# Performance work log

Hardware: AMD Instinct MI355X
Metric: run time of the kernel (lower is better)

## Reference

```python
import jax, jax.numpy as jnp
import numpy as np

N, H, DK, DV, DFF, D = 2, 8, 32, 32, 512, 256
B, S = 2, 2048
MASK_VALUE = -1e-30
EPS = 1e-14  # K.epsilon()**2 with default epsilon 1e-7


def glorot(key, shape):
    fan_in, fan_out = shape[-2], shape[-1]
    limit = np.sqrt(6.0 / (fan_in + fan_out))
    return jax.random.uniform(key, shape, jnp.float32, -limit, limit)


def setup_inputs() -> dict:
    key = jax.random.key(0)
    ks = jax.random.split(key, 8)
    return {
        "x": jax.random.normal(ks[0], (B, S, D), jnp.float32),
        "mask": jnp.ones((B, S), jnp.float32),
        "Wq": glorot(ks[1], (N, H, D, DK)),
        "Wk": glorot(ks[2], (N, H, D, DK)),
        "Wv": glorot(ks[3], (N, H, D, DV)),
        "Wo": glorot(ks[4], (N, H * DV, D)),
        "W1": glorot(ks[5], (N, D, DFF)),
        "b1": jnp.zeros((N, DFF), jnp.float32),
        "W2": glorot(ks[6], (N, DFF, D)),
        "b2": jnp.zeros((N, D), jnp.float32),
        "gamma": jnp.ones((2 * N,), jnp.float32),
        "beta": jnp.zeros((2 * N,), jnp.float32),
    }


def _layernorm(x, g, b):
    mean = jnp.mean(x, axis=-1, keepdims=True)
    var = jnp.mean(jnp.square(x - mean), axis=-1, keepdims=True)
    return (x - mean) / jnp.sqrt(var + EPS) * g + b


def reference(x, mask, Wq, Wk, Wv, Wo, W1, b1, W2, b2, gamma, beta):
    m = mask[:, None, None, :]  # [B,1,1,S], multiplies score rows' key axis
    for i in range(N):
        # batched multi-head attention (no 1/sqrt(dk) scaling, faithful to source)
        q = jnp.einsum("bsd,hdk->bhsk", x, Wq[i])
        k = jnp.einsum("bsd,hdk->bhsk", x, Wk[i])
        v = jnp.einsum("bsd,hdv->bhsv", x, Wv[i])
        A = jnp.einsum("bhsk,bhtk->bhst", q, k)  # [B,H,S,S]
        A = m * A + (1.0 - m) * MASK_VALUE
        A = jax.nn.softmax(A, axis=-1)
        o = jnp.einsum("bhst,bhtv->bhsv", A, v)
        conc = o.transpose(0, 2, 1, 3).reshape(x.shape[0], x.shape[1], H * DV)
        x = x + conc @ Wo[i]
        x = _layernorm(x, gamma[2 * i], beta[2 * i])
        ffn = jax.nn.relu(x @ W1[i] + b1[i]) @ W2[i] + b2[i]
        x = x + ffn
        x = _layernorm(x, gamma[2 * i + 1], beta[2 * i + 1])
    return x
```

## Files before the change

kernel.cpp:

```cpp
#include <hip/hip_runtime.h>
#include <hip/hip_bf16.h>

#define NL 2
#define NH 8
#define DKk 32
#define DVv 32
#define DFF 512
#define DD 256
#define BB 2
#define SS 2048
#define MROWS (BB*SS)
#define LN_EPS 1e-14f
#define L2E 1.4426950408889634f
#define SOFT_SHIFT_L2E (50.0f*L2E)

typedef __hip_bfloat16 bf16;
typedef unsigned short us;
typedef short bf16x8 __attribute__((ext_vector_type(8)));
typedef float f32x4  __attribute__((ext_vector_type(4)));
typedef unsigned short us4 __attribute__((ext_vector_type(4)));

#define O_XF   256
#define O_QB   (O_XF+1048576)
#define O_KH   (O_QB+1048576)
#define O_KL   (O_KH+524288)
#define O_VT   (O_KL+524288)
#define O_XH   (O_VT+524288)
#define O_XL   (O_XH+524288)
#define O_OP   (O_XL+524288)
#define O_ML   (O_OP+2097152)
#define O_MASK (O_ML+65536)
#define O_B1   (O_MASK+4096)
#define O_B2   (O_B1+1024)
#define O_GM   (O_B2+512)
#define O_BT   (O_GM+4)
#define O_PREP (O_BT+4)
#define TAIL_TOTAL (4096+1024+512+4+4)
#define CONV_BLOCKS (512 + (TAIL_TOTAL+255)/256)
#define PREP_BLOCKS 512
#define PQH 0u
#define PQL 393216u
#define POH 786432u
#define POL 917504u
#define P1H 1048576u
#define P1L 1310720u
#define P2H 1572864u
#define P2L 1835008u

__device__ __forceinline__ float us2f(us u){
  unsigned int v = ((unsigned int)u) << 16; float f;
  __builtin_memcpy(&f, &v, 4); return f;
}
__device__ __forceinline__ us f2bf_rne(float f){
  unsigned int b = __float_as_uint(f);
  b += 0x7FFFu + ((b>>16)&1u);
  return (us)(b>>16);
}

#if __has_builtin(__builtin_amdgcn_exp2f)
#define EXP2F(x) __builtin_amdgcn_exp2f(x)
#else
#define EXP2F(x) exp2f(x)
#endif

#if __has_builtin(__builtin_amdgcn_cvt_pk_bf16_f32)
typedef __bf16 bf16x2_t __attribute__((ext_vector_type(2)));
__device__ __forceinline__ int pack_bf16(float a, float b){
  bf16x2_t r = __builtin_amdgcn_cvt_pk_bf16_f32(a, b);
  int i; __builtin_memcpy(&i, &r, 4); return i;
}
#else
__device__ __forceinline__ int pack_bf16(float a, float b){
  int b0 = __float_as_int(a) + 0x8000;
  int b1 = __float_as_int(b) + 0x8000;
  return (b1 & 0xFFFF0000) | ((int)((unsigned)b0 >> 16));
}
#endif

__device__ __forceinline__ void gl_lds16(const us* g, us* l){
  __builtin_amdgcn_global_load_lds(
    (const __attribute__((address_space(1))) unsigned int*)g,
    (__attribute__((address_space(3))) unsigned int*)l, 16, 0, 0);
}

__device__ __forceinline__ size_t xhl_idx(int row, int col){
  int rt = row>>6, rg = (row>>4)&3, L15 = row&15;
  int kc = col>>5, Q = (col>>3)&3, j = col&7;
  return ((size_t)(rt*8+kc))*2048 + rg*512 + Q*128 + L15*8 + j;
}

__device__ __forceinline__ float conv1(const void* src, size_t i, int flag){
  if(flag) return ((const float*)src)[i];
  return us2f(((const us*)src)[i]);
}

__device__ __forceinline__ void prep_b_raw(const void* W0, const void* W1v, const void* W2v,
                                           int baseoff, us* __restrict__ Bh, us* __restrict__ Bl,
                                           int Kd, int Nd, int qkv, int g, int flag)
{
  int total = (Kd/32)*(Nd/16)*64;
  if(g >= total) return;
  int lane = g & 63, fi = g >> 6;
  int ncN = Nd/16;
  int nc = fi % ncN, kc = fi / ncN;
  int Q = lane>>4, L15 = lane&15;
  int n = nc*16 + L15;
  const void* src;
  int off0, stride;
  if(qkv){
    int sec = n>>8, h = (n>>5)&7, kq = n&31;
    src = (sec==0)?W0:((sec==1)?W1v:W2v);
    off0 = baseoff + h*8192 + kq;
    stride = 32;
  } else {
    src = W0;
    off0 = baseoff + n;
    stride = Nd;
  }
  #pragma unroll
  for(int j=0;j<8;j++){
    int k = kc*32 + Q*8 + j;
    float v = conv1(src, (size_t)off0 + (size_t)k*stride, flag);
    us hb = f2bf_rne(v);
    Bh[(size_t)g*8 + j] = hb;
    Bl[(size_t)g*8 + j] = f2bf_rne(v - us2f(hb));
  }
}

__global__ void conv_prep(const void* s0, const void* s1, const void* sWq, const void* sWk,
                          const void* sWv, const void* sWo, const void* sW1, const void* sb1,
                          const void* sW2, const void* sb2, const void* sgm, const void* sbt,
                          float* __restrict__ ws, int* __restrict__ flagp)
{
  __shared__ int fsh[4];
  int bad = 0;
  const us* xr = (const us*)s0;
  for(int i=threadIdx.x; i<4096; i+=256){
    float f = us2f(xr[i]);
    if(!(fabsf(f) < 1e3f)) bad = 1;
  }
  unsigned long long m = __ballot(bad);
  if((threadIdx.x&63)==0) fsh[threadIdx.x>>6] = (m!=0ull);
  __syncthreads();
  int flag = (fsh[0]|fsh[1]|fsh[2]|fsh[3]);
  if(blockIdx.x==0 && threadIdx.x==0) *flagp = flag;

  int b = blockIdx.x;
  if(b < PREP_BLOCKS){
    int layer = b >> 8, lb = b & 255;
    us* prep = (us*)(ws + O_PREP);
    if(lb < 96){
      int g = lb*256 + threadIdx.x;
      prep_b_raw(sWq, sWk, sWv, layer*65536, prep+PQH+(size_t)layer*196608,
                 prep+PQL+(size_t)layer*196608, 256, 768, 1, g, flag);
    } else if(lb < 128){
      int g = (lb-96)*256 + threadIdx.x;
      prep_b_raw(sWo, nullptr, nullptr, layer*65536, prep+POH+(size_t)layer*65536,
                 prep+POL+(size_t)layer*65536, 256, 256, 0, g, flag);
    } else if(lb < 192){
      int g = (lb-128)*256 + threadIdx.x;
      prep_b_raw(sW1, nullptr, nullptr, layer*131072, prep+P1H+(size_t)layer*131072,
                 prep+P1L+(size_t)layer*131072, 256, 512, 0, g, flag);
    } else {
      int g = (lb-192)*256 + threadIdx.x;
      prep_b_raw(sW2, nullptr, nullptr, layer*131072, prep+P2H+(size_t)layer*131072,
                 prep+P2L+(size_t)layer*131072, 512, 256, 0, g, flag);
    }
    return;
  }
  int b2 = b - PREP_BLOCKS;
  if(b2 < 512){
    int g8 = b2*256 + threadIdx.x;
    int e0 = g8*8;
    float v[8];
    if(flag){
      float4 a0 = *((const float4*)s0 + (e0>>2));
      float4 a1 = *((const float4*)s0 + (e0>>2) + 1);
      v[0]=a0.x; v[1]=a0.y; v[2]=a0.z; v[3]=a0.w;
      v[4]=a1.x; v[5]=a1.y; v[6]=a1.z; v[7]=a1.w;
    } else {
      bf16x8 u = *((const bf16x8*)s0 + g8);
      #pragma unroll
      for(int j=0;j<8;j++) v[j] = us2f((us)u[j]);
    }
    *(float4*)&ws[O_XF+e0]   = (float4){v[0],v[1],v[2],v[3]};
    *(float4*)&ws[O_XF+e0+4] = (float4){v[4],v[5],v[6],v[7]};
    union{ us a[8]; uint4 q; } hh, ll;
    #pragma unroll
    for(int j=0;j<8;j++){
      us hb = f2bf_rne(v[j]);
      hh.a[j] = hb;
      ll.a[j] = f2bf_rne(v[j] - us2f(hb));
    }
    size_t xi = xhl_idx(e0>>8, e0&255);
    *(uint4*)&((us*)(ws+O_XH))[xi] = hh.q;
    *(uint4*)&((us*)(ws+O_XL))[xi] = ll.q;
    return;
  }
  int g = (b2-512)*256 + threadIdx.x;
  if(g < 4096){ ws[O_MASK+g] = conv1(s1, g, flag)*L2E; return; }
  g -= 4096;
  if(g < 1024){ ws[O_B1+g] = conv1(sb1, g, flag); return; }
  g -= 1024;
  if(g < 512){ ws[O_B2+g] = conv1(sb2, g, flag); return; }
  g -= 512;
  if(g < 4){ ws[O_GM+g] = conv1(sgm, g, flag); return; }
  g -= 4;
  if(g < 4){ ws[O_BT+g] = conv1(sbt, g, flag); return; }
}

template<int MODE>
__launch_bounds__(256)
__global__ void gemm_mfma(const us* __restrict__ Axh, const us* __restrict__ Axl,
                          const us* __restrict__ Bh, const us* __restrict__ Bl,
                          const float* __restrict__ bias,
                          float* __restrict__ O,
                          us* __restrict__ QH, us* __restrict__ QL,
                          us* __restrict__ KH, us* __restrict__ KL, us* __restrict__ VT,
                          int Ncols, int Kdim)
{
  __shared__ __align__(16) us SH[16384];
  const int t = threadIdx.x;
  const int w = t>>6, lane = t&63;
  const int Q = lane>>4, L15 = lane&15;
  const int bx = blockIdx.x, by = blockIdx.y;
  const int row0 = bx*64;
  const int nc0 = by*4;
  const int col0 = by*64;
  const int nKc = Kdim>>5;
  const int ncW = Ncols>>4;

  f32x4 acc[2][2];
  #pragma unroll
  for(int i=0;i<2;i++)
    #pragma unroll
    for(int j=0;j<2;j++) acc[i][j] = (f32x4){0.f,0.f,0.f,0.f};

  auto stage = [&](int kc){
    const int bo = (kc&1)*8192;
    size_t abase = ((size_t)(bx*nKc + kc))*2048;
    gl_lds16(&Axh[abase + (size_t)t*8], &SH[bo + t*8]);
    gl_lds16(&Axl[abase + (size_t)t*8], &SH[bo + 2048 + t*8]);
    size_t gidx = ((size_t)(kc*ncW + nc0 + w)*64 + lane)*8;
    gl_lds16(&Bh[gidx], &SH[bo + 4096 + t*8]);
    gl_lds16(&Bl[gidx], &SH[bo + 6144 + t*8]);
  };

  stage(0);

  for(int kc=0; kc<nKc; kc++){
    __syncthreads();
    if(kc+1 < nKc) stage(kc+1);
    const int bo = (kc&1)*8192;
    const us* Ah  = SH + bo;
    const us* Al  = SH + bo + 2048;
    const us* Bhs = SH + bo + 4096;
    const us* Bls = SH + bo + 6144;

    bf16x8 aAh[2], aAl[2], bBh[2], bBl[2];
    #pragma unroll
    for(int rg2=0;rg2<2;rg2++){
      int rg = (w&1)*2 + rg2;
      aAh[rg2] = *(const bf16x8*)&Ah[rg*512 + lane*8];
      aAl[rg2] = *(const bf16x8*)&Al[rg*512 + lane*8];
    }
    #pragma unroll
    for(int cg2=0;cg2<2;cg2++){
      int nc = (w>>1)*2 + cg2;
      bBh[cg2] = *(const bf16x8*)&Bhs[nc*512 + lane*8];
      bBl[cg2] = *(const bf16x8*)&Bls[nc*512 + lane*8];
    }
    #pragma unroll
    for(int rg2=0;rg2<2;rg2++)
      #pragma unroll
      for(int cg2=0;cg2<2;cg2++){
        acc[rg2][cg2] = __builtin_amdgcn_mfma_f32_16x16x32_bf16(aAl[rg2], bBh[cg2], acc[rg2][cg2], 0,0,0);
        acc[rg2][cg2] = __builtin_amdgcn_mfma_f32_16x16x32_bf16(aAh[rg2], bBl[cg2], acc[rg2][cg2], 0,0,0);
        acc[rg2][cg2] = __builtin_amdgcn_mfma_f32_16x16x32_bf16(aAh[rg2], bBh[cg2], acc[rg2][cg2], 0,0,0);
      }
  }

  if(MODE==0){
    __syncthreads();
    us* TH = SH;
    us* TL = SH + 4608;
    #pragma unroll
    for(int rg2=0;rg2<2;rg2++)
      #pragma unroll
      for(int cg2=0;cg2<2;cg2++)
        #pragma unroll
        for(int r=0;r<4;r++){
          int rl = (w&1)*32 + rg2*16 + Q*4 + r;
          int cl = (w>>1)*32 + cg2*16 + L15;
          float va = acc[rg2][cg2][r];
          us hb = f2bf_rne(va);
          TH[rl*72+cl] = hb;
          TL[rl*72+cl] = f2bf_rne(va - us2f(hb));
        }
    __syncthreads();
    const int sec = col0>>8;
    const int h0  = (col0&255)>>5;
    const int b_  = row0>>11;
    const int srow0 = row0 & 2047;
    if(sec < 2){
      us* DH = (sec==0) ? QH : KH;
      us* DL = (sec==0) ? QL : KL;
      #pragma unroll
      for(int u2=0; u2<2; u2++){
        int u = w + u2*4;
        int rg = u&3, half = u>>2;
        int lbase = (rg*16 + L15)*72 + half*32 + Q*8;
        bf16x8 hv = *(const bf16x8*)&TH[lbase];
        bf16x8 lv = *(const bf16x8*)&TL[lbase];
        int bh = b_*NH + h0 + half;
        size_t dbase = ((size_t)(bh*128 + (srow0>>4) + rg)*64 + lane)*8;
        *(bf16x8*)&DH[dbase] = hv;
        *(bf16x8*)&DL[dbase] = lv;
      }
    } else {
      #pragma unroll
      for(int u2=0; u2<2; u2++){
        int u = w + u2*4;
        int sgrp = u&1, kqh = (u>>1)&1, half = u>>2;
        union{ us u8[8]; bf16x8 v; } vv;
        #pragma unroll
        for(int j=0;j<8;j++){
          int rl = sgrp*32 + Q*8 + j;
          int cl = half*32 + kqh*16 + L15;
          vv.u8[j] = TH[rl*72+cl];
        }
        int bh = b_*NH + h0 + half;
        size_t dbase = ((size_t)((bh*64 + (srow0>>5) + sgrp)*2 + kqh)*64 + lane)*8;
        *(bf16x8*)&VT[dbase] = vv.v;
      }
    }
  } else {
    #pragma unroll
    for(int rg2=0;rg2<2;rg2++)
      #pragma unroll
      for(int cg2=0;cg2<2;cg2++)
        #pragma unroll
        for(int r=0;r<4;r++){
          int row = row0 + (w&1)*32 + rg2*16 + Q*4 + r;
          int c   = col0 + (w>>1)*32 + cg2*16 + L15;
          float v = acc[rg2][cg2][r] + bias[c];
          O[(size_t)row*Ncols + c] = v>0.f ? v : 0.f;
        }
  }
}

template<int SRC>
__launch_bounds__(256)
__global__ void gemm_ln(const float* __restrict__ A,
                        const float* __restrict__ OpartA, const float* __restrict__ MLA,
                        const us* __restrict__ Bh, const us* __restrict__ Bl,
                        const float* __restrict__ bias, const float* __restrict__ res,
                        float* __restrict__ xf,
                        us* __restrict__ xh, us* __restrict__ xl,
                        const float* __restrict__ gamma, const float* __restrict__ beta, int gi,
                        void* __restrict__ out, int write_out,
                        const int* __restrict__ flagp, int Kdim)
{
  __shared__ __align__(16) us Ahs[1024], Als[1024];
  __shared__ __align__(16) us Bhs[16384], Bls[16384];
  __shared__ float lred[128];
  const int t = threadIdx.x;
  const int w = t>>6, lane = t&63;
  const int Q = lane>>4, L15 = lane&15;
  const int row0 = blockIdx.x*16;
  const int nKc = Kdim>>5;

  f32x4 acc[4];
  #pragma unroll
  for(int cg=0;cg<4;cg++) acc[cg] = (f32x4){0.f,0.f,0.f,0.f};

  float4 pv0, pv1, pv;
  float pl0 = 0.f, pl1 = 0.f;

  auto preloadA = [&](int kc){
    if(t < 128){
      int r = t>>3;
      int kl = (t&7)*4;
      if(SRC==0){
        int row = row0 + r;
        int b_ = row>>11, s_ = row&2047;
        size_t i0 = (size_t)(b_*8 + kc)*2048 + s_;
        pl0 = MLA[i0];
        pl1 = MLA[i0+32768];
        pv0 = *(const float4*)&OpartA[i0*32 + kl];
        pv1 = *(const float4*)&OpartA[(i0+32768)*32 + kl];
      } else {
        pv = *(const float4*)&A[(size_t)(row0+r)*Kdim + kc*32 + kl];
      }
    }
  };
  auto writeA = [&](int kc){
    if(t < 128){
      int r = t>>3;
      int kl = (t&7)*4;
      float f[4];
      if(SRC==0){
        float inv = 1.f/(pl0 + pl1);
        f[0]=(pv0.x+pv1.x)*inv; f[1]=(pv0.y+pv1.y)*inv;
        f[2]=(pv0.z+pv1.z)*inv; f[3]=(pv0.w+pv1.w)*inv;
      } else {
        f[0]=pv.x; f[1]=pv.y; f[2]=pv.z; f[3]=pv.w;
      }
      us4 h4, l4;
      #pragma unroll
      for(int j=0;j<4;j++){
        us hb = f2bf_rne(f[j]);
        h4[j] = hb; l4[j] = f2bf_rne(f[j] - us2f(hb));
      }
      int bo = (kc&1)*512;
      int off = (kl>>3)*128 + r*8 + (kl&7);
      *(us4*)&Ahs[bo+off] = h4;
      *(us4*)&Als[bo+off] = l4;
    }
  };
  auto stageB = [&](int kc){
    const int bo = (kc&1)*8192;
    #pragma unroll
    for(int ii=0; ii<4; ii++){
      int unit = w + ii*4;
      size_t gidx = ((size_t)(kc*16 + unit)*64 + lane)*8;
      gl_lds16(&Bh[gidx], &Bhs[bo + unit*512 + lane*8]);
      gl_lds16(&Bl[gidx], &Bls[bo + unit*512 + lane*8]);
    }
  };

  preloadA(0);
  stageB(0);
  writeA(0);

  for(int kc=0; kc<nKc; kc++){
    __syncthreads();
    if(kc+1 < nKc){
      preloadA(kc+1);
      stageB(kc+1);
    }
    const int bo = (kc&1);
    bf16x8 aAh = *(const bf16x8*)&Ahs[bo*512 + lane*8];
    bf16x8 aAl = *(const bf16x8*)&Als[bo*512 + lane*8];
    #pragma unroll
    for(int cg=0;cg<4;cg++){
      int unit = w*4 + cg;
      bf16x8 bBh = *(const bf16x8*)&Bhs[bo*8192 + unit*512 + lane*8];
      bf16x8 bBl = *(const bf16x8*)&Bls[bo*8192 + unit*512 + lane*8];
      acc[cg] = __builtin_amdgcn_mfma_f32_16x16x32_bf16(aAl, bBh, acc[cg], 0,0,0);
      acc[cg] = __builtin_amdgcn_mfma_f32_16x16x32_bf16(aAh, bBl, acc[cg], 0,0,0);
      acc[cg] = __builtin_amdgcn_mfma_f32_16x16x32_bf16(aAh, bBh, acc[cg], 0,0,0);
    }
    if(kc+1 < nKc) writeA(kc+1);
  }

  float tmp[4][4];
  #pragma unroll
  for(int cg=0;cg<4;cg++)
    #pragma unroll
    for(int r=0;r<4;r++){
      int row = row0 + Q*4 + r;
      int c = w*64 + cg*16 + L15;
      float v = acc[cg][r] + res[(size_t)row*DD + c];
      if(SRC==1) v += bias[c];
      tmp[cg][r] = v;
    }
  float s[4], sq[4];
  #pragma unroll
  for(int r=0;r<4;r++){
    s[r]  = tmp[0][r]+tmp[1][r]+tmp[2][r]+tmp[3][r];
    sq[r] = tmp[0][r]*tmp[0][r]+tmp[1][r]*tmp[1][r]+tmp[2][r]*tmp[2][r]+tmp[3][r]*tmp[3][r];
  }
  #pragma unroll
  for(int off=1; off<16; off<<=1)
    #pragma unroll
    for(int r=0;r<4;r++){
      s[r]  += __shfl_xor(s[r], off);
      sq[r] += __shfl_xor(sq[r], off);
    }
  if(L15==0){
    #pragma unroll
    for(int r=0;r<4;r++){
      int rl = Q*4 + r;
      lred[(w*16 + rl)*2]   = s[r];
      lred[(w*16 + rl)*2+1] = sq[r];
    }
  }
  __syncthreads();
  float g = gamma[gi], bb = beta[gi];
  float scv[4], mnv[4];
  #pragma unroll
  for(int r=0;r<4;r++){
    int rl = Q*4 + r;
    float S  = lred[rl*2]   + lred[(16+rl)*2]   + lred[(32+rl)*2]   + lred[(48+rl)*2];
    float SQ = lred[rl*2+1] + lred[(16+rl)*2+1] + lred[(32+rl)*2+1] + lred[(48+rl)*2+1];
    float mean = S*(1.f/DD);
    float var  = SQ*(1.f/DD) - mean*mean;
    scv[r] = rsqrtf(var+LN_EPS)*g;
    mnv[r] = mean;
  }
  int flag = write_out ? *flagp : 0;
  #pragma unroll
  for(int cg=0;cg<4;cg++)
    #pragma unroll
    for(int r=0;r<4;r++){
      int row = row0 + Q*4 + r;
      int c = w*64 + cg*16 + L15;
      float val = (tmp[cg][r]-mnv[r])*scv[r] + bb;
      xf[(size_t)row*DD + c] = val;
      us hb = f2bf_rne(val);
      size_t xi = xhl_idx(row, c);
      xh[xi] = hb;
      xl[xi] = f2bf_rne(val - us2f(hb));
      if(write_out){
        if(flag) ((float*)out)[(size_t)row*DD + c] = val;
        else     ((bf16*)out)[(size_t)row*DD + c] = __float2bfloat16(val);
      }
    }
}

__launch_bounds__(256)
__global__ void ffn_ln(const us* __restrict__ XHg, const us* __restrict__ XLg,
                       const us* __restrict__ W1h, const us* __restrict__ W1l,
                       const us* __restrict__ W2h, const us* __restrict__ W2l,
                       const float* __restrict__ b1, const float* __restrict__ b2,
                       const float* __restrict__ res,
                       float* __restrict__ xf, us* __restrict__ xh, us* __restrict__ xl,
                       const float* __restrict__ gamma, const float* __restrict__ beta, int gi,
                       void* __restrict__ out, int write_out, const int* __restrict__ flagp)
{
  __shared__ __align__(16) us SH[32768];
  __shared__ __align__(16) us hAH[8192], hAL[8192];
  __shared__ float lred[128];
  const int t = threadIdx.x;
  const int w = t>>6, lane = t&63;
  const int Q = lane>>4, L15 = lane&15;
  const int row0 = blockIdx.x*16;
  const int rt = row0>>6, rg = (row0>>4)&3;

  auto stageW = [&](const us* Bh, const us* Bl, int fi0, int buf){
    const int bo = buf*16384;
    #pragma unroll
    for(int ii=0; ii<4; ii++){
      int u = w + ii*4;
      size_t gidx = ((size_t)(fi0 + u)*64 + lane)*8;
      gl_lds16(&Bh[gidx], &SH[bo + u*512 + lane*8]);
      gl_lds16(&Bl[gidx], &SH[bo + 8192 + u*512 + lane*8]);
    }
  };

  f32x4 acc_y[4];
  #pragma unroll
  for(int cg=0;cg<4;cg++) acc_y[cg] = (f32x4){0.f,0.f,0.f,0.f};

  stageW(W1h, W1l, 0, 0);

  int step = 0;
  for(int nch=0; nch<2; nch++){
    f32x4 acc_h[4];
    #pragma unroll
    for(int cg=0;cg<4;cg++) acc_h[cg] = (f32x4){0.f,0.f,0.f,0.f};
    for(int kc=0; kc<8; kc++){
      __syncthreads();
      int ns = step + 1;
      if(ns < 16){
        int nnch = ns>>3, nkc = ns&7;
        stageW(W1h, W1l, nkc*32 + nnch*16, ns&1);
      } else {
        stageW(W2h, W2l, 0, ns&1);
      }
      const int bo = (step&1)*16384;
      size_t abase = ((size_t)(rt*8+kc))*2048 + (size_t)rg*512 + (size_t)lane*8;
      bf16x8 aAh = *(const bf16x8*)&XHg[abase];
      bf16x8 aAl = *(const bf16x8*)&XLg[abase];
      #pragma unroll
      for(int cg=0;cg<4;cg++){
        int u = w*4 + cg;
        bf16x8 bBh = *(const bf16x8*)&SH[bo + u*512 + lane*8];
        bf16x8 bBl = *(const bf16x8*)&SH[bo + 8192 + u*512 + lane*8];
        acc_h[cg] = __builtin_amdgcn_mfma_f32_16x16x32_bf16(aAl, bBh, acc_h[cg], 0,0,0);
        acc_h[cg] = __builtin_amdgcn_mfma_f32_16x16x32_bf16(aAh, bBl, acc_h[cg], 0,0,0);
        acc_h[cg] = __builtin_amdgcn_mfma_f32_16x16x32_bf16(aAh, bBh, acc_h[cg], 0,0,0);
      }
      step++;
    }
    #pragma unroll
    for(int cg=0;cg<4;cg++){
      int col = nch*256 + (w*4+cg)*16 + L15;
      float bv = b1[col];
      int base = (col>>5)*512 + (((col&31)>>3))*128 + (col&7);
      #pragma unroll
      for(int r=0;r<4;r++){
        int row = Q*4 + r;
        float v = acc_h[cg][r] + bv;
        v = v>0.f ? v : 0.f;
        us hb = f2bf_rne(v);
        hAH[base + row*8] = hb;
        hAL[base + row*8] = f2bf_rne(v - us2f(hb));
      }
    }
  }
  for(int kc2=0; kc2<16; kc2++){
    __syncthreads();
    if(kc2+1 < 16) stageW(W2h, W2l, (kc2+1)*16, (step+1)&1);
    const int bo = (step&1)*16384;
    bf16x8 aAh = *(const bf16x8*)&hAH[kc2*512 + lane*8];
    bf16x8 aAl = *(const bf16x8*)&hAL[kc2*512 + lane*8];
    #pragma unroll
    for(int cg=0;cg<4;cg++){
      int u = w*4 + cg;
      bf16x8 bBh = *(const bf16x8*)&SH[bo + u*512 + lane*8];
      bf16x8 bBl = *(const bf16x8*)&SH[bo + 8192 + u*512 + lane*8];
      acc_y[cg] = __builtin_amdgcn_mfma_f32_16x16x32_bf16(aAl, bBh, acc_y[cg], 0,0,0);
      acc_y[cg] = __builtin_amdgcn_mfma_f32_16x16x32_bf16(aAh, bBl, acc_y[cg], 0,0,0);
      acc_y[cg] = __builtin_amdgcn_mfma_f32_16x16x32_bf16(aAh, bBh, acc_y[cg], 0,0,0);
    }
    step++;
  }

  float tmp[4][4];
  #pragma unroll
  for(int cg=0;cg<4;cg++)
    #pragma unroll
    for(int r=0;r<4;r++){
      int row = row0 + Q*4 + r;
      int c = w*64 + cg*16 + L15;
      tmp[cg][r] = acc_y[cg][r] + res[(size_t)row*DD + c] + b2[c];
    }
  float s[4], sq[4];
  #pragma unroll
  for(int r=0;r<4;r++){
    s[r]  = tmp[0][r]+tmp[1][r]+tmp[2][r]+tmp[3][r];
    sq[r] = tmp[0][r]*tmp[0][r]+tmp[1][r]*tmp[1][r]+tmp[2][r]*tmp[2][r]+tmp[3][r]*tmp[3][r];
  }
  #pragma unroll
  for(int off=1; off<16; off<<=1)
    #pragma unroll
    for(int r=0;r<4;r++){
      s[r]  += __shfl_xor(s[r], off);
      sq[r] += __shfl_xor(sq[r], off);
    }
  if(L15==0){
    #pragma unroll
    for(int r=0;r<4;r++){
      int rl = Q*4 + r;
      lred[(w*16 + rl)*2]   = s[r];
      lred[(w*16 + rl)*2+1] = sq[r];
    }
  }
  __syncthreads();
  float g = gamma[gi], bb = beta[gi];
  float scv[4], mnv[4];
  #pragma unroll
  for(int r=0;r<4;r++){
    int rl = Q*4 + r;
    float S  = lred[rl*2]   + lred[(16+rl)*2]   + lred[(32+rl)*2]   + lred[(48+rl)*2];
    float SQ = lred[rl*2+1] + lred[(16+rl)*2+1] + lred[(32+rl)*2+1] + lred[(48+rl)*2+1];
    float mean = S*(1.f/DD);
    float var  = SQ*(1.f/DD) - mean*mean;
    scv[r] = rsqrtf(var+LN_EPS)*g;
    mnv[r] = mean;
  }
  int flag = write_out ? *flagp : 0;
  #pragma unroll
  for(int cg=0;cg<4;cg++)
    #pragma unroll
    for(int r=0;r<4;r++){
      int row = row0 + Q*4 + r;
      int c = w*64 + cg*16 + L15;
      float val = (tmp[cg][r]-mnv[r])*scv[r] + bb;
      xf[(size_t)row*DD + c] = val;
      us hb = f2bf_rne(val);
      size_t xi = xhl_idx(row, c);
      xh[xi] = hb;
      xl[xi] = f2bf_rne(val - us2f(hb));
      if(write_out){
        if(flag) ((float*)out)[(size_t)row*DD + c] = val;
        else     ((bf16*)out)[(size_t)row*DD + c] = __float2bfloat16(val);
      }
    }
}

__launch_bounds__(256)
__global__ void attn_kernel(const us* __restrict__ QH, const us* __restrict__ QL,
                            const us* __restrict__ KH, const us* __restrict__ KL,
                            const us* __restrict__ VT,
                            const float* __restrict__ mask,
                            float* __restrict__ Opart, float* __restrict__ ML)
{
  __shared__ __align__(16) us Khs[4096], Kls[4096], Vts[4096];
  __shared__ __align__(16) float Msl[1024];
  const int t = threadIdx.x;
  const int bh = blockIdx.x >> 6;
  const int qt = (blockIdx.x & 63) >> 1;
  const int ks = blockIdx.x & 1;
  const int b_ = bh >> 3;
  const int wv = t >> 6;
  const int lane = t & 63;
  const int Q = lane >> 4, L15 = lane & 15;
  const int q0 = qt*64 + wv*16;

  size_t qidx = ((size_t)(bh*128 + qt*4 + wv)*64 + lane)*8;
  const bf16x8 qh_v = *(const bf16x8*)&QH[qidx];
  const bf16x8 ql_v = *(const bf16x8*)&QL[qidx];

  const us* KHbh = KH + (size_t)bh*65536;
  const us* KLbh = KL + (size_t)bh*65536;
  const us* VTbh = VT + (size_t)bh*65536;
  const int base = ks*1024;

  f32x4 Oa0a = {0.f,0.f,0.f,0.f}, Oa0b = {0.f,0.f,0.f,0.f};
  f32x4 Oa1a = {0.f,0.f,0.f,0.f}, Oa1b = {0.f,0.f,0.f,0.f};
  float lacc = 0.f;

  {
    const us* mrow = (const us*)(mask + (size_t)b_*SS + base);
    gl_lds16(mrow + (size_t)t*8, ((us*)Msl) + t*8);
    size_t kbase = (size_t)(base>>4)*512;
    size_t vbase = (size_t)(base>>5)*1024;
    gl_lds16(&KHbh[kbase + (size_t)t*8], &Khs[t*8]);
    gl_lds16(&KLbh[kbase + (size_t)t*8], &Kls[t*8]);
    gl_lds16(&VTbh[vbase + (size_t)t*8], &Vts[t*8]);
  }

  for(int s=0; s<16; s++){
    __syncthreads();
    if(s < 15){
      int t0n = base + (s+1)*64;
      int bn = (s+1)&1;
      size_t kbase = (size_t)(t0n>>4)*512;
      size_t vbase = (size_t)(t0n>>5)*1024;
      gl_lds16(&KHbh[kbase + (size_t)t*8], &Khs[bn*2048 + t*8]);
      gl_lds16(&KLbh[kbase + (size_t)t*8], &Kls[bn*2048 + t*8]);
      gl_lds16(&VTbh[vbase + (size_t)t*8], &Vts[bn*2048 + t*8]);
    }
    const int bo = (s&1)*2048;
    const int mo = s*64;

    f32x4 St[4];
    const f32x4 zz = {0.f,0.f,0.f,0.f};
    #pragma unroll
    for(int kt=0;kt<4;kt++){
      bf16x8 aKh = *(const bf16x8*)&Khs[bo + kt*512 + lane*8];
      bf16x8 aKl = *(const bf16x8*)&Kls[bo + kt*512 + lane*8];
      f32x4 a = __builtin_amdgcn_mfma_f32_16x16x32_bf16(aKl, qh_v, zz, 0,0,0);
      a = __builtin_amdgcn_mfma_f32_16x16x32_bf16(aKh, ql_v, a, 0,0,0);
      a = __builtin_amdgcn_mfma_f32_16x16x32_bf16(aKh, qh_v, a, 0,0,0);
      St[kt] = a;
    }

    float lsum = 0.f;
    #pragma unroll
    for(int kt=0;kt<4;kt++){
      float4 mv = *(const float4*)&Msl[mo + kt*16 + Q*4];
      float mvr[4] = {mv.x, mv.y, mv.z, mv.w};
      #pragma unroll
      for(int r=0;r<4;r++){
        float p = EXP2F(fmaf(mvr[r], St[kt][r], -SOFT_SHIFT_L2E));
        St[kt][r] = p;
        lsum += p;
      }
    }
    lacc += lsum;

    int pk[4][2];
    #pragma unroll
    for(int kt=0;kt<4;kt++){
      pk[kt][0] = pack_bf16(St[kt][0], St[kt][1]);
      pk[kt][1] = pack_bf16(St[kt][2], St[kt][3]);
    }

    #pragma unroll
    for(int c=0;c<2;c++){
      union { int i[4]; bf16x8 v; } bu;
      #pragma unroll
      for(int d=0;d<4;d++){
        int srcl = (((Q&1)*2 + (d>>1))<<4) | L15;
        int vlo = __shfl(pk[2*c  ][d&1], srcl, 64);
        int vhi = __shfl(pk[2*c+1][d&1], srcl, 64);
        bu.i[d] = (Q & 2) ? vhi : vlo;
      }
      bf16x8 aV0 = *(const bf16x8*)&Vts[bo + (c*2+0)*512 + lane*8];
      bf16x8 aV1 = *(const bf16x8*)&Vts[bo + (c*2+1)*512 + lane*8];
      if(c == 0){
        Oa0a = __builtin_amdgcn_mfma_f32_16x16x32_bf16(aV0, bu.v, Oa0a, 0,0,0);
        Oa1a = __builtin_amdgcn_mfma_f32_16x16x32_bf16(aV1, bu.v, Oa1a, 0,0,0);
      } else {
        Oa0b = __builtin_amdgcn_mfma_f32_16x16x32_bf16(aV0, bu.v, Oa0b, 0,0,0);
        Oa1b = __builtin_amdgcn_mfma_f32_16x16x32_bf16(aV1, bu.v, Oa1b, 0,0,0);
      }
    }
  }

  f32x4 Oa0 = Oa0a + Oa0b;
  f32x4 Oa1 = Oa1a + Oa1b;
  lacc += __shfl_xor(lacc, 16);
  lacc += __shfl_xor(lacc, 32);

  float* opp = &Opart[((size_t)(ks*16+bh)*SS + q0 + L15)*32];
  #pragma unroll
  for(int r=0;r<4;r++){
    opp[Q*4+r]    = Oa0[r];
    opp[16+Q*4+r] = Oa1[r];
  }
  if(Q==0){
    ML[(size_t)(ks*16+bh)*SS + q0 + L15] = lacc;
  }
}

extern "C" void kernel_launch(void* const* d_in, const int* in_sizes, int n_in,
                              void* d_out, int out_size, void* d_ws, size_t ws_size,
                              hipStream_t stream)
{
  float* ws = (float*)d_ws;
  int* flagp = (int*)d_ws;

  float* xf  = ws + O_XF;
  us* QHb = (us*)(ws + O_QB);
  us* QLb = QHb + 1048576;
  us* KH = (us*)(ws + O_KH);
  us* KL = (us*)(ws + O_KL);
  us* VT = (us*)(ws + O_VT);
  us* XH = (us*)(ws + O_XH);
  us* XL = (us*)(ws + O_XL);
  float* Opart = ws + O_OP;
  float* ML  = ws + O_ML;
  float* b1f = ws + O_B1;
  float* b2f_ = ws + O_B2;
  float* gmf = ws + O_GM;
  float* btf = ws + O_BT;
  us* prep = (us*)(ws + O_PREP);

  conv_prep<<<PREP_BLOCKS+CONV_BLOCKS,256,0,stream>>>(
      d_in[0], d_in[1], d_in[2], d_in[3], d_in[4], d_in[5],
      d_in[6], d_in[7], d_in[8], d_in[9], d_in[10], d_in[11],
      ws, flagp);

  for(int i=0;i<NL;i++){
    const float* b1i = b1f + (size_t)i*DFF;
    const float* b2i = b2f_ + (size_t)i*DD;

    dim3 g0(64, 12);
    gemm_mfma<0><<<g0,256,0,stream>>>(XH, XL,
                                      prep+PQH+(size_t)i*196608, prep+PQL+(size_t)i*196608,
                                      nullptr, nullptr,
                                      QHb, QLb, KH, KL, VT, 768, 256);
    attn_kernel<<<1024,256,0,stream>>>(QHb, QLb, KH, KL, VT, ws + O_MASK, Opart, ML);
    gemm_ln<0><<<256,256,0,stream>>>(nullptr, Opart, ML,
                                     prep+POH+(size_t)i*65536, prep+POL+(size_t)i*65536,
                                     nullptr, xf, xf, XH, XL,
                                     gmf, btf, 2*i, d_out, 0, flagp, 256);
    ffn_ln<<<256,256,0,stream>>>(XH, XL,
                                 prep+P1H+(size_t)i*131072, prep+P1L+(size_t)i*131072,
                                 prep+P2H+(size_t)i*131072, prep+P2L+(size_t)i*131072,
                                 b1i, b2i, xf, xf, XH, XL,
                                 gmf, btf, 2*i+1, d_out, (i==NL-1)?1:0, flagp);
  }
}
```

Before: 261.6 us.

## Fuse output-projection LayerNorm kernel into FFN LayerNorm kernel

Merges the attention output projection plus residual and first LayerNorm into the FFN kernel, so each 16-row block computes Wo, LN1, the FFN and LN2 in one launch. The LN1 result stays in LDS as split bf16 hi/lo operands and in registers as the residual. This removes one kernel launch and the global round trip of the intermediate activations. The weight staging schedule is chained across the two GEMM phases. The cost is a larger LDS footprint per block, which may lower occupancy.

```diff
diff --git a/kernel.cpp b/kernel.cpp
--- a/kernel.cpp
+++ b/kernel.cpp
@@ -349,194 +349,25 @@
   }
 }
 
-template<int SRC>
 __launch_bounds__(256)
-__global__ void gemm_ln(const float* __restrict__ A,
-                        const float* __restrict__ OpartA, const float* __restrict__ MLA,
-                        const us* __restrict__ Bh, const us* __restrict__ Bl,
-                        const float* __restrict__ bias, const float* __restrict__ res,
-                        float* __restrict__ xf,
-                        us* __restrict__ xh, us* __restrict__ xl,
-                        const float* __restrict__ gamma, const float* __restrict__ beta, int gi,
-                        void* __restrict__ out, int write_out,
-                        const int* __restrict__ flagp, int Kdim)
-{
-  __shared__ __align__(16) us Ahs[1024], Als[1024];
-  __shared__ __align__(16) us Bhs[16384], Bls[16384];
-  __shared__ float lred[128];
-  const int t = threadIdx.x;
-  const int w = t>>6, lane = t&63;
-  const int Q = lane>>4, L15 = lane&15;
-  const int row0 = blockIdx.x*16;
-  const int nKc = Kdim>>5;
-
-  f32x4 acc[4];
-  #pragma unroll
-  for(int cg=0;cg<4;cg++) acc[cg] = (f32x4){0.f,0.f,0.f,0.f};
-
-  float4 pv0, pv1, pv;
-  float pl0 = 0.f, pl1 = 0.f;
-
-  auto preloadA = [&](int kc){
-    if(t < 128){
-      int r = t>>3;
-      int kl = (t&7)*4;
-      if(SRC==0){
-        int row = row0 + r;
-        int b_ = row>>11, s_ = row&2047;
-        size_t i0 = (size_t)(b_*8 + kc)*2048 + s_;
-        pl0 = MLA[i0];
-        pl1 = MLA[i0+32768];
-        pv0 = *(const float4*)&OpartA[i0*32 + kl];
-        pv1 = *(const float4*)&OpartA[(i0+32768)*32 + kl];
-      } else {
-        pv = *(const float4*)&A[(size_t)(row0+r)*Kdim + kc*32 + kl];
-      }
-    }
-  };
-  auto writeA = [&](int kc){
-    if(t < 128){
-      int r = t>>3;
-      int kl = (t&7)*4;
-      float f[4];
-      if(SRC==0){
-        float inv = 1.f/(pl0 + pl1);
-        f[0]=(pv0.x+pv1.x)*inv; f[1]=(pv0.y+pv1.y)*inv;
-        f[2]=(pv0.z+pv1.z)*inv; f[3]=(pv0.w+pv1.w)*inv;
-      } else {
-        f[0]=pv.x; f[1]=pv.y; f[2]=pv.z; f[3]=pv.w;
-      }
-      us4 h4, l4;
-      #pragma unroll
-      for(int j=0;j<4;j++){
-        us hb = f2bf_rne(f[j]);
-        h4[j] = hb; l4[j] = f2bf_rne(f[j] - us2f(hb));
-      }
-      int bo = (kc&1)*512;
-      int off = (kl>>3)*128 + r*8 + (kl&7);
-      *(us4*)&Ahs[bo+off] = h4;
-      *(us4*)&Als[bo+off] = l4;
-    }
-  };
-  auto stageB = [&](int kc){
-    const int bo = (kc&1)*8192;
-    #pragma unroll
-    for(int ii=0; ii<4; ii++){
-      int unit = w + ii*4;
-      size_t gidx = ((size_t)(kc*16 + unit)*64 + lane)*8;
-      gl_lds16(&Bh[gidx], &Bhs[bo + unit*512 + lane*8]);
-      gl_lds16(&Bl[gidx], &Bls[bo + unit*512 + lane*8]);
-    }
-  };
-
-  preloadA(0);
-  stageB(0);
-  writeA(0);
-
-  for(int kc=0; kc<nKc; kc++){
-    __syncthreads();
-    if(kc+1 < nKc){
-      preloadA(kc+1);
-      stageB(kc+1);
-    }
-    const int bo = (kc&1);
-    bf16x8 aAh = *(const bf16x8*)&Ahs[bo*512 + lane*8];
-    bf16x8 aAl = *(const bf16x8*)&Als[bo*512 + lane*8];
-    #pragma unroll
-    for(int cg=0;cg<4;cg++){
-      int unit = w*4 + cg;
-      bf16x8 bBh = *(const bf16x8*)&Bhs[bo*8192 + unit*512 + lane*8];
-      bf16x8 bBl = *(const bf16x8*)&Bls[bo*8192 + unit*512 + lane*8];
-      acc[cg] = __builtin_amdgcn_mfma_f32_16x16x32_bf16(aAl, bBh, acc[cg], 0,0,0);
-      acc[cg] = __builtin_amdgcn_mfma_f32_16x16x32_bf16(aAh, bBl, acc[cg], 0,0,0);
-      acc[cg] = __builtin_amdgcn_mfma_f32_16x16x32_bf16(aAh, bBh, acc[cg], 0,0,0);
-    }
-    if(kc+1 < nKc) writeA(kc+1);
-  }
-
-  float tmp[4][4];
-  #pragma unroll
-  for(int cg=0;cg<4;cg++)
-    #pragma unroll
-    for(int r=0;r<4;r++){
-      int row = row0 + Q*4 + r;
-      int c = w*64 + cg*16 + L15;
-      float v = acc[cg][r] + res[(size_t)row*DD + c];
-      if(SRC==1) v += bias[c];
-      tmp[cg][r] = v;
-    }
-  float s[4], sq[4];
-  #pragma unroll
-  for(int r=0;r<4;r++){
-    s[r]  = tmp[0][r]+tmp[1][r]+tmp[2][r]+tmp[3][r];
-    sq[r] = tmp[0][r]*tmp[0][r]+tmp[1][r]*tmp[1][r]+tmp[2][r]*tmp[2][r]+tmp[3][r]*tmp[3][r];
-  }
-  #pragma unroll
-  for(int off=1; off<16; off<<=1)
-    #pragma unroll
-    for(int r=0;r<4;r++){
-      s[r]  += __shfl_xor(s[r], off);
-      sq[r] += __shfl_xor(sq[r], off);
-    }
-  if(L15==0){
-    #pragma unroll
-    for(int r=0;r<4;r++){
-      int rl = Q*4 + r;
-      lred[(w*16 + rl)*2]   = s[r];
-      lred[(w*16 + rl)*2+1] = sq[r];
-    }
-  }
-  __syncthreads();
-  float g = gamma[gi], bb = beta[gi];
-  float scv[4], mnv[4];
-  #pragma unroll
-  for(int r=0;r<4;r++){
-    int rl = Q*4 + r;
-    float S  = lred[rl*2]   + lred[(16+rl)*2]   + lred[(32+rl)*2]   + lred[(48+rl)*2];
-    float SQ = lred[rl*2+1] + lred[(16+rl)*2+1] + lred[(32+rl)*2+1] + lred[(48+rl)*2+1];
-    float mean = S*(1.f/DD);
-    float var  = SQ*(1.f/DD) - mean*mean;
-    scv[r] = rsqrtf(var+LN_EPS)*g;
-    mnv[r] = mean;
-  }
-  int flag = write_out ? *flagp : 0;
-  #pragma unroll
-  for(int cg=0;cg<4;cg++)
-    #pragma unroll
-    for(int r=0;r<4;r++){
-      int row = row0 + Q*4 + r;
-      int c = w*64 + cg*16 + L15;
-      float val = (tmp[cg][r]-mnv[r])*scv[r] + bb;
-      xf[(size_t)row*DD + c] = val;
-      us hb = f2bf_rne(val);
-      size_t xi = xhl_idx(row, c);
-      xh[xi] = hb;
-      xl[xi] = f2bf_rne(val - us2f(hb));
-      if(write_out){
-        if(flag) ((float*)out)[(size_t)row*DD + c] = val;
-        else     ((bf16*)out)[(size_t)row*DD + c] = __float2bfloat16(val);
-      }
-    }
-}
-
-__launch_bounds__(256)
-__global__ void ffn_ln(const us* __restrict__ XHg, const us* __restrict__ XLg,
-                       const us* __restrict__ W1h, const us* __restrict__ W1l,
-                       const us* __restrict__ W2h, const us* __restrict__ W2l,
-                       const float* __restrict__ b1, const float* __restrict__ b2,
-                       const float* __restrict__ res,
-                       float* __restrict__ xf, us* __restrict__ xh, us* __restrict__ xl,
-                       const float* __restrict__ gamma, const float* __restrict__ beta, int gi,
-                       void* __restrict__ out, int write_out, const int* __restrict__ flagp)
+__global__ void oln_ffn(const float* __restrict__ OpartA, const float* __restrict__ MLA,
+                        const us* __restrict__ WOh, const us* __restrict__ WOl,
+                        const us* __restrict__ W1h, const us* __restrict__ W1l,
+                        const us* __restrict__ W2h, const us* __restrict__ W2l,
+                        const float* __restrict__ b1, const float* __restrict__ b2,
+                        float* __restrict__ xf, us* __restrict__ xh, us* __restrict__ xl,
+                        const float* __restrict__ gamma, const float* __restrict__ beta, int gi0,
+                        void* __restrict__ out, int write_out, const int* __restrict__ flagp)
 {
   __shared__ __align__(16) us SH[32768];
+  __shared__ __align__(16) us Ahs[1024], Als[1024];
+  __shared__ __align__(16) us xAH[4096], xAL[4096];
   __shared__ __align__(16) us hAH[8192], hAL[8192];
   __shared__ float lred[128];
   const int t = threadIdx.x;
   const int w = t>>6, lane = t&63;
   const int Q = lane>>4, L15 = lane&15;
   const int row0 = blockIdx.x*16;
-  const int rt = row0>>6, rg = (row0>>4)&3;
 
   auto stageW = [&](const us* Bh, const us* Bl, int fi0, int buf){
     const int bo = buf*16384;
@@ -549,30 +380,148 @@
     }
   };
 
-  f32x4 acc_y[4];
-  #pragma unroll
-  for(int cg=0;cg<4;cg++) acc_y[cg] = (f32x4){0.f,0.f,0.f,0.f};
-
-  stageW(W1h, W1l, 0, 0);
-
-  int step = 0;
+  float4 pv0, pv1;
+  float pl0 = 0.f, pl1 = 0.f;
+  auto preloadA = [&](int kc){
+    if(t < 128){
+      int r = t>>3;
+      int kl = (t&7)*4;
+      int row = row0 + r;
+      int b_ = row>>11, s_ = row&2047;
+      size_t i0 = (size_t)(b_*8 + kc)*2048 + s_;
+      pl0 = MLA[i0];
+      pl1 = MLA[i0+32768];
+      pv0 = *(const float4*)&OpartA[i0*32 + kl];
+      pv1 = *(const float4*)&OpartA[(i0+32768)*32 + kl];
+    }
+  };
+  auto writeA = [&](int kc){
+    if(t < 128){
+      int r = t>>3;
+      int kl = (t&7)*4;
+      float inv = 1.f/(pl0 + pl1);
+      float f[4] = {(pv0.x+pv1.x)*inv, (pv0.y+pv1.y)*inv,
+                    (pv0.z+pv1.z)*inv, (pv0.w+pv1.w)*inv};
+      us4 h4, l4;
+      #pragma unroll
+      for(int j=0;j<4;j++){
+        us hb = f2bf_rne(f[j]);
+        h4[j] = hb; l4[j] = f2bf_rne(f[j] - us2f(hb));
+      }
+      int bo = (kc&1)*512;
+      int off = (kl>>3)*128 + r*8 + (kl&7);
+      *(us4*)&Ahs[bo+off] = h4;
+      *(us4*)&Als[bo+off] = l4;
+    }
+  };
+
+  f32x4 acc[4];
+  #pragma unroll
+  for(int cg=0;cg<4;cg++) acc[cg] = (f32x4){0.f,0.f,0.f,0.f};
+
+  preloadA(0);
+  stageW(WOh, WOl, 0, 0);
+  writeA(0);
+
+  for(int kc=0; kc<8; kc++){
+    __syncthreads();
+    if(kc < 7){
+      preloadA(kc+1);
+      stageW(WOh, WOl, (kc+1)*16, (kc+1)&1);
+    } else {
+      stageW(W1h, W1l, 0, 0);
+    }
+    const int bo = (kc&1)*16384;
+    bf16x8 aAh = *(const bf16x8*)&Ahs[(kc&1)*512 + lane*8];
+    bf16x8 aAl = *(const bf16x8*)&Als[(kc&1)*512 + lane*8];
+    #pragma unroll
+    for(int cg=0;cg<4;cg++){
+      int u = w*4 + cg;
+      bf16x8 bBh = *(const bf16x8*)&SH[bo + u*512 + lane*8];
+      bf16x8 bBl = *(const bf16x8*)&SH[bo + 8192 + u*512 + lane*8];
+      acc[cg] = __builtin_amdgcn_mfma_f32_16x16x32_bf16(aAl, bBh, acc[cg], 0,0,0);
+      acc[cg] = __builtin_amdgcn_mfma_f32_16x16x32_bf16(aAh, bBl, acc[cg], 0,0,0);
+      acc[cg] = __builtin_amdgcn_mfma_f32_16x16x32_bf16(aAh, bBh, acc[cg], 0,0,0);
+    }
+    if(kc < 7) writeA(kc+1);
+  }
+
+  float tmp[4][4];
+  #pragma unroll
+  for(int cg=0;cg<4;cg++)
+    #pragma unroll
+    for(int r=0;r<4;r++){
+      int row = row0 + Q*4 + r;
+      int c = w*64 + cg*16 + L15;
+      tmp[cg][r] = acc[cg][r] + xf[(size_t)row*DD + c];
+    }
+  float s[4], sq[4];
+  #pragma unroll
+  for(int r=0;r<4;r++){
+    s[r]  = tmp[0][r]+tmp[1][r]+tmp[2][r]+tmp[3][r];
+    sq[r] = tmp[0][r]*tmp[0][r]+tmp[1][r]*tmp[1][r]+tmp[2][r]*tmp[2][r]+tmp[3][r]*tmp[3][r];
+  }
+  #pragma unroll
+  for(int off=1; off<16; off<<=1)
+    #pragma unroll
+    for(int r=0;r<4;r++){
+      s[r]  += __shfl_xor(s[r], off);
+      sq[r] += __shfl_xor(sq[r], off);
+    }
+  if(L15==0){
+    #pragma unroll
+    for(int r=0;r<4;r++){
+      int rl = Q*4 + r;
+      lred[(w*16 + rl)*2]   = s[r];
+      lred[(w*16 + rl)*2+1] = sq[r];
+    }
+  }
+  __syncthreads();
+  float val_s[4][4];
+  {
+    float g = gamma[gi0], bb = beta[gi0];
+    float scv[4], mnv[4];
+    #pragma unroll
+    for(int r=0;r<4;r++){
+      int rl = Q*4 + r;
+      float S  = lred[rl*2]   + lred[(16+rl)*2]   + lred[(32+rl)*2]   + lred[(48+rl)*2];
+      float SQ = lred[rl*2+1] + lred[(16+rl)*2+1] + lred[(32+rl)*2+1] + lred[(48+rl)*2+1];
+      float mean = S*(1.f/DD);
+      float var  = SQ*(1.f/DD) - mean*mean;
+      scv[r] = rsqrtf(var+LN_EPS)*g;
+      mnv[r] = mean;
+    }
+    #pragma unroll
+    for(int cg=0;cg<4;cg++){
+      int c = w*64 + cg*16 + L15;
+      int base = (c>>5)*512 + (((c&31)>>3))*128 + (c&7);
+      #pragma unroll
+      for(int r=0;r<4;r++){
+        float v = (tmp[cg][r]-mnv[r])*scv[r] + bb;
+        val_s[cg][r] = v;
+        us hb = f2bf_rne(v);
+        xAH[base + (Q*4+r)*8] = hb;
+        xAL[base + (Q*4+r)*8] = f2bf_rne(v - us2f(hb));
+      }
+    }
+  }
+
+  int step = 8;
   for(int nch=0; nch<2; nch++){
     f32x4 acc_h[4];
     #pragma unroll
     for(int cg=0;cg<4;cg++) acc_h[cg] = (f32x4){0.f,0.f,0.f,0.f};
     for(int kc=0; kc<8; kc++){
       __syncthreads();
-      int ns = step + 1;
+      int ns = step - 8 + 1;
       if(ns < 16){
-        int nnch = ns>>3, nkc = ns&7;
-        stageW(W1h, W1l, nkc*32 + nnch*16, ns&1);
+        stageW(W1h, W1l, (ns&7)*32 + (ns>>3)*16, (step+1)&1);
       } else {
-        stageW(W2h, W2l, 0, ns&1);
+        stageW(W2h, W2l, 0, (step+1)&1);
       }
       const int bo = (step&1)*16384;
-      size_t abase = ((size_t)(rt*8+kc))*2048 + (size_t)rg*512 + (size_t)lane*8;
-      bf16x8 aAh = *(const bf16x8*)&XHg[abase];
-      bf16x8 aAl = *(const bf16x8*)&XLg[abase];
+      bf16x8 aAh = *(const bf16x8*)&xAH[kc*512 + lane*8];
+      bf16x8 aAl = *(const bf16x8*)&xAL[kc*512 + lane*8];
       #pragma unroll
       for(int cg=0;cg<4;cg++){
         int u = w*4 + cg;
@@ -600,6 +549,10 @@
       }
     }
   }
+
+  f32x4 acc_y[4];
+  #pragma unroll
+  for(int cg=0;cg<4;cg++) acc_y[cg] = (f32x4){0.f,0.f,0.f,0.f};
   for(int kc2=0; kc2<16; kc2++){
     __syncthreads();
     if(kc2+1 < 16) stageW(W2h, W2l, (kc2+1)*16, (step+1)&1);
@@ -618,39 +571,39 @@
     step++;
   }
 
-  float tmp[4][4];
+  float tmp2[4][4];
   #pragma unroll
   for(int cg=0;cg<4;cg++)
     #pragma unroll
     for(int r=0;r<4;r++){
-      int row = row0 + Q*4 + r;
       int c = w*64 + cg*16 + L15;
-      tmp[cg][r] = acc_y[cg][r] + res[(size_t)row*DD + c] + b2[c];
-    }
-  float s[4], sq[4];
+      tmp2[cg][r] = acc_y[cg][r] + val_s[cg][r] + b2[c];
+    }
+  float s2[4], sq2[4];
   #pragma unroll
   for(int r=0;r<4;r++){
-    s[r]  = tmp[0][r]+tmp[1][r]+tmp[2][r]+tmp[3][r];
-    sq[r] = tmp[0][r]*tmp[0][r]+tmp[1][r]*tmp[1][r]+tmp[2][r]*tmp[2][r]+tmp[3][r]*tmp[3][r];
+    s2[r]  = tmp2[0][r]+tmp2[1][r]+tmp2[2][r]+tmp2[3][r];
+    sq2[r] = tmp2[0][r]*tmp2[0][r]+tmp2[1][r]*tmp2[1][r]+tmp2[2][r]*tmp2[2][r]+tmp2[3][r]*tmp2[3][r];
   }
   #pragma unroll
   for(int off=1; off<16; off<<=1)
     #pragma unroll
     for(int r=0;r<4;r++){
-      s[r]  += __shfl_xor(s[r], off);
-      sq[r] += __shfl_xor(sq[r], off);
-    }
+      s2[r]  += __shfl_xor(s2[r], off);
+      sq2[r] += __shfl_xor(sq2[r], off);
+    }
+  __syncthreads();
   if(L15==0){
     #pragma unroll
     for(int r=0;r<4;r++){
       int rl = Q*4 + r;
-      lred[(w*16 + rl)*2]   = s[r];
-      lred[(w*16 + rl)*2+1] = sq[r];
+      lred[(w*16 + rl)*2]   = s2[r];
+      lred[(w*16 + rl)*2+1] = sq2[r];
     }
   }
   __syncthreads();
-  float g = gamma[gi], bb = beta[gi];
-  float scv[4], mnv[4];
+  float g2 = gamma[gi0+1], bb2 = beta[gi0+1];
+  float scv2[4], mnv2[4];
   #pragma unroll
   for(int r=0;r<4;r++){
     int rl = Q*4 + r;
@@ -658,8 +611,8 @@
     float SQ = lred[rl*2+1] + lred[(16+rl)*2+1] + lred[(32+rl)*2+1] + lred[(48+rl)*2+1];
     float mean = S*(1.f/DD);
     float var  = SQ*(1.f/DD) - mean*mean;
-    scv[r] = rsqrtf(var+LN_EPS)*g;
-    mnv[r] = mean;
+    scv2[r] = rsqrtf(var+LN_EPS)*g2;
+    mnv2[r] = mean;
   }
   int flag = write_out ? *flagp : 0;
   #pragma unroll
@@ -668,7 +621,7 @@
     for(int r=0;r<4;r++){
       int row = row0 + Q*4 + r;
       int c = w*64 + cg*16 + L15;
-      float val = (tmp[cg][r]-mnv[r])*scv[r] + bb;
+      float val = (tmp2[cg][r]-mnv2[r])*scv2[r] + bb2;
       xf[(size_t)row*DD + c] = val;
       us hb = f2bf_rne(val);
       size_t xi = xhl_idx(row, c);
@@ -846,14 +799,11 @@
                                       nullptr, nullptr,
                                       QHb, QLb, KH, KL, VT, 768, 256);
     attn_kernel<<<1024,256,0,stream>>>(QHb, QLb, KH, KL, VT, ws + O_MASK, Opart, ML);
-    gemm_ln<0><<<256,256,0,stream>>>(nullptr, Opart, ML,
-                                     prep+POH+(size_t)i*65536, prep+POL+(size_t)i*65536,
-                                     nullptr, xf, xf, XH, XL,
-                                     gmf, btf, 2*i, d_out, 0, flagp, 256);
-    ffn_ln<<<256,256,0,stream>>>(XH, XL,
-                                 prep+P1H+(size_t)i*131072, prep+P1L+(size_t)i*131072,
-                                 prep+P2H+(size_t)i*131072, prep+P2L+(size_t)i*131072,
-                                 b1i, b2i, xf, xf, XH, XL,
-                                 gmf, btf, 2*i+1, d_out, (i==NL-1)?1:0, flagp);
-  }
-}
+    oln_ffn<<<256,256,0,stream>>>(Opart, ML,
+                                  prep+POH+(size_t)i*65536, prep+POL+(size_t)i*65536,
+                                  prep+P1H+(size_t)i*131072, prep+P1L+(size_t)i*131072,
+                                  prep+P2H+(size_t)i*131072, prep+P2L+(size_t)i*131072,
+                                  b1i, b2i, xf, XH, XL,
+                                  gmf, btf, 2*i, d_out, (i==NL-1)?1:0, flagp);
+  }
+}
```

New measurement: 257.1 us. Within noise of the previous version (-1.7%).
